# Kernel optimization log

Measured on AMD Instinct MI355X. Metric: run time of the kernel, lower is better.

## Reference

```python
import jax, jax.numpy as jnp
import numpy as np

N_USERS = 90000
N_ITEMS = 60000
N = N_USERS + N_ITEMS   # 150000 total nodes
D = 64                  # emb_dim
K = 128                 # n_intents
E = 1600000             # directed edges
L = 3                   # n_layers
EPS = 1e-12


def setup_inputs() -> dict:
    key = jax.random.key(0)
    k0, k1, k2, k3, k4 = jax.random.split(key, 5)
    embeddings = jax.random.normal(k0, (N, D), dtype=jnp.float32) * 0.1
    user_intent = jax.random.normal(k1, (D, K), dtype=jnp.float32) * 0.1
    item_intent = jax.random.normal(k2, (D, K), dtype=jnp.float32) * 0.1
    all_h = jax.random.randint(k3, (E,), 0, N, dtype=jnp.int32)
    all_t = jax.random.randint(k4, (E,), 0, N, dtype=jnp.int32)
    return {"embeddings": embeddings, "user_intent": user_intent,
            "item_intent": item_intent, "all_h": all_h, "all_t": all_t}


def _spmm(vals, h, t, x):
    # y[i] = sum_{e: h[e]==i} vals[e] * x[t[e]]   (sparse adj @ x)
    return jax.ops.segment_sum(vals[:, None] * x[t], h, num_segments=N)


def _sym_norm_values(h, t):
    # G = D^{-1/2} A D^{-1/2} edge values (A has unit edge weights)
    deg = jax.ops.segment_sum(jnp.ones((E,), jnp.float32), h, num_segments=N)
    d_inv = jnp.where(deg > 0, deg ** -0.5, 0.0)
    return d_inv[h] * d_inv[t]


def _adaptive_values(head_emb, tail_emb, h):
    # F.normalize: x / max(||x||, eps)
    hn = head_emb / jnp.maximum(jnp.linalg.norm(head_emb, axis=1, keepdims=True), EPS)
    tn = tail_emb / jnp.maximum(jnp.linalg.norm(tail_emb, axis=1, keepdims=True), EPS)
    edge_alpha = (jnp.sum(hn * tn, axis=1) + 1.0) * 0.5          # [E]
    row_sum = jax.ops.segment_sum(edge_alpha, h, num_segments=N)  # degree scores
    d_inv = jnp.where(row_sum > 0, 1.0 / row_sum, 0.0)           # pow(-1).nan_to_num
    return d_inv[h] * edge_alpha


def reference(embeddings, user_intent, item_intent, all_h, all_t):
    g_vals = _sym_norm_values(all_h, all_t)
    x = embeddings
    acc = x  # sum over all layer embeddings (incl. layer 0)
    for _ in range(L):
        gnn = _spmm(g_vals, all_h, all_t, x)
        u, it = x[:N_USERS], x[N_USERS:]
        u_int = jax.nn.softmax(u @ user_intent, axis=1) @ user_intent.T
        i_int = jax.nn.softmax(it @ item_intent, axis=1) @ item_intent.T
        intl = jnp.concatenate([u_int, i_int], axis=0)            # [N, D]
        gaa_vals = _adaptive_values(gnn[all_h], gnn[all_t], all_h)
        iaa_vals = _adaptive_values(intl[all_h], intl[all_t], all_h)
        gaa = _spmm(gaa_vals, all_h, all_t, x)
        iaa = _spmm(iaa_vals, all_h, all_t, x)
        x = gnn + intl + gaa + iaa + x
        acc = acc + x
    return acc
```

## Files before the change

### kernel.cpp

```cpp
#include <hip/hip_runtime.h>

#define N_USERS 90000
#define N_ITEMS 60000
#define NN      (N_USERS + N_ITEMS)
#define D       64
#define KDIM    128
#define NE      1600000
#define EPSF    1e-12f
#define ROWD    64
#define TU      ((N_USERS + 63) / 64)
#define TI      ((N_ITEMS + 63) / 64)
#define NINT    (TU + TI)
#define GB      4096


typedef __fp16 h2 __attribute__((ext_vector_type(2)));
typedef __fp16 h8 __attribute__((ext_vector_type(8)));
typedef float  f2 __attribute__((ext_vector_type(2)));
typedef float  f4v __attribute__((ext_vector_type(4)));

__device__ inline h2 as_h2(unsigned u) {
    union { unsigned u; h2 h; } v; v.u = u; return v.h;
}
__device__ inline h8 as_h8(uint4 u) {
    union { uint4 u; h8 h; } v; v.u = u; return v.h;
}
__device__ inline unsigned pkrtz(float a, float b) {
    auto r = __builtin_amdgcn_cvt_pkrtz(a, b);
    union { decltype(r) h; unsigned u; } v; v.h = r; return v.u;
}
__device__ inline f2 dec8lo(unsigned u) {
    return __builtin_amdgcn_cvt_pk_f32_fp8((int)u, false);
}
__device__ inline f2 dec8hi(unsigned u) {
    return __builtin_amdgcn_cvt_pk_f32_fp8((int)u, true);
}
__device__ inline unsigned enc8(float a, float b, float c, float d) {
    int u = __builtin_amdgcn_cvt_pk_fp8_f32(a, b, 0, false);
    u = __builtin_amdgcn_cvt_pk_fp8_f32(c, d, u, true);
    return (unsigned)u;
}


#define EB   ((NE + 255) / 256)
#define IB   ((NN * 16 + 255) / 256)
#define PREG (EB + IB + 16)

__global__ void k_pre(const int* __restrict__ h, int* __restrict__ deg,
                      const float* __restrict__ emb,
                      float* __restrict__ acc, unsigned* __restrict__ pkA,
                      const float* __restrict__ Wu, const float* __restrict__ Wi,
                      uint4* __restrict__ WfA, uint4* __restrict__ Wf2) {
    int bid = blockIdx.x;
    if (bid < EB) {
        int e = bid * 256 + threadIdx.x;
        if (e < NE) atomicAdd(&deg[h[e]], 1);
    } else if (bid < EB + IB) {
        int i = (bid - EB) * 256 + threadIdx.x;
        if (i >= NN * 16) return;
        float4 v = ((const float4*)emb)[i];
        ((float4*)acc)[i] = v;
        int row = i >> 4, l = i & 15;
        *(uint2*)&pkA[(size_t)row * ROWD + 32 + 2 * l] =
            make_uint2(pkrtz(v.x, v.y), pkrtz(v.z, v.w));
    } else {
        int i = (bid - EB - IB) * 256 + threadIdx.x;
        if (i >= 4096) return;
        int ph  = i >> 11;
        int r   = i & 2047;
        int mat = r >> 10;
        int rr  = r & 1023;
        const float* W = mat ? Wi : Wu;
        union { __fp16 hh[8]; uint4 u; } pkt;
        if (!ph) {
            int nt = rr >> 7, ks = (rr >> 6) & 1, lane = rr & 63;
            int q = lane >> 4, c = lane & 15;
            #pragma unroll
            for (int j = 0; j < 8; ++j)
                pkt.hh[j] = (__fp16)W[(32 * ks + 8 * q + j) * KDIM + nt * 16 + c];
            WfA[((mat * 8 + nt) * 2 + ks) * 64 + lane] = pkt.u;
        } else {
            int nt = rr >> 8, ks = (rr >> 6) & 3, lane = rr & 63;
            int q = lane >> 4, c = lane & 15;
            #pragma unroll
            for (int j = 0; j < 8; ++j)
                pkt.hh[j] = (__fp16)W[(nt * 16 + c) * KDIM + 32 * ks + 8 * q + j];
            Wf2[((mat * 4 + nt) * 4 + ks) * 64 + lane] = pkt.u;
        }
    }
}

__global__ void k_rowoff(const int* __restrict__ deg, int* __restrict__ counter,
                         int* __restrict__ row_off, int2* __restrict__ rodeg,
                         float* __restrict__ d_inv) {
    int i = blockIdx.x * blockDim.x + threadIdx.x;
    if (i >= NN) return;
    int d = deg[i];
    int ro = atomicAdd(counter, d);
    row_off[i] = ro;
    rodeg[i]   = make_int2(ro, d);
    d_inv[i]   = (d > 0) ? rsqrtf((float)d) : 0.f;
}

__global__ void k_scatter(const int* __restrict__ h, const int* __restrict__ t,
                          const int* __restrict__ row_off, int* __restrict__ row_cur,
                          const float* __restrict__ d_inv,
                          int2* __restrict__ csr) {
    int e = blockIdx.x * blockDim.x + threadIdx.x;
    if (e >= NE) return;
    int hh = h[e], tt = t[e];
    int slot = row_off[hh] + atomicAdd(&row_cur[hh], 1);
    csr[slot] = make_int2(tt, __float_as_int(d_inv[hh] * d_inv[tt]));
}

__global__ __launch_bounds__(256) void k_mid(const int2* __restrict__ rodeg,
                                             const int2* __restrict__ csr,
                                             unsigned* __restrict__ pk,
                                             unsigned* __restrict__ intl_h,
                                             const uint4* __restrict__ WfA,
                                             const uint4* __restrict__ Wf2,
                                             unsigned* __restrict__ base16) {
    __shared__ unsigned Plds[4096];
    int tid = threadIdx.x;
    int bid = blockIdx.x;

    if (bid < NINT) {
        int mat, bse, count, n0;
        if (bid < TU) { mat = 0; bse = 0;       count = N_USERS; n0 = bid * 64; }
        else          { mat = 1; bse = N_USERS; count = N_ITEMS; n0 = (bid - TU) * 64; }

        int wv = tid >> 6, la = tid & 63;
        int q = la >> 4, c = la & 15;

        int nA = n0 + wv * 16 + c;
        size_t gA = (size_t)min(bse + nA, NN - 1);
        const unsigned* prA = pk + gA * ROWD;
        uint4 a0u = *(const uint4*)&prA[32 + 4 * q];
        uint4 a1u = *(const uint4*)&prA[48 + 4 * q];

        f4v S[8];
        #pragma unroll
        for (int nt = 0; nt < 8; ++nt) S[nt] = (f4v){0.f, 0.f, 0.f, 0.f};
        const uint4* WA = WfA + (size_t)mat * 1024;
        #pragma unroll
        for (int nt = 0; nt < 8; ++nt) {
            h8 B0 = as_h8(WA[(nt * 2 + 0) * 64 + la]);
            h8 B1 = as_h8(WA[(nt * 2 + 1) * 64 + la]);
            S[nt] = __builtin_amdgcn_mfma_f32_16x16x32_f16(as_h8(a0u), B0, S[nt], 0, 0, 0);
            S[nt] = __builtin_amdgcn_mfma_f32_16x16x32_f16(as_h8(a1u), B1, S[nt], 0, 0, 0);
        }

        float inv_s[4];
        #pragma unroll
        for (int reg = 0; reg < 4; ++reg) {
            float m = S[0][reg];
            #pragma unroll
            for (int nt = 1; nt < 8; ++nt) m = fmaxf(m, S[nt][reg]);
            m = fmaxf(m, __shfl_xor(m, 1)); m = fmaxf(m, __shfl_xor(m, 2));
            m = fmaxf(m, __shfl_xor(m, 4)); m = fmaxf(m, __shfl_xor(m, 8));
            float sm = 0.f;
            #pragma unroll
            for (int nt = 0; nt < 8; ++nt) {
                float e_ = __expf(S[nt][reg] - m);
                S[nt][reg] = e_;
                sm += e_;
            }
            sm += __shfl_xor(sm, 1); sm += __shfl_xor(sm, 2);
            sm += __shfl_xor(sm, 4); sm += __shfl_xor(sm, 8);
            inv_s[reg] = 1.f / sm;
        }

        #pragma unroll
        for (int reg = 0; reg < 4; ++reg) {
            int ln = wv * 16 + q * 4 + reg;
            #pragma unroll
            for (int nt = 0; nt < 8; ++nt) {
                float v  = S[nt][reg] * inv_s[reg];
                float v1 = __shfl_xor(v, 1);
                if (!(c & 1)) {
                    int byte_in_row = nt * 32 + c * 2;
                    int sw = byte_in_row ^ ((ln & 7) << 4);
                    *(unsigned*)((char*)Plds + ln * 256 + sw) = pkrtz(v, v1);
                }
            }
        }

        f4v O[4];
        #pragma unroll
        for (int nt = 0; nt < 4; ++nt) O[nt] = (f4v){0.f, 0.f, 0.f, 0.f};
        const uint4* W2 = Wf2 + (size_t)mat * 1024;
        int lnA = wv * 16 + c;
        #pragma unroll
        for (int ks = 0; ks < 4; ++ks) {
            int byte_in_row = (32 * ks + 8 * q) * 2;
            int sw = byte_in_row ^ ((lnA & 7) << 4);
            uint4 au = *(const uint4*)((char*)Plds + lnA * 256 + sw);
            #pragma unroll
            for (int nt = 0; nt < 4; ++nt) {
                h8 Bp = as_h8(W2[(nt * 4 + ks) * 64 + la]);
                O[nt] = __builtin_amdgcn_mfma_f32_16x16x32_f16(as_h8(au), Bp, O[nt], 0, 0, 0);
            }
        }

        #pragma unroll
        for (int reg = 0; reg < 4; ++reg) {
            float ss = 0.f;
            #pragma unroll
            for (int nt = 0; nt < 4; ++nt) ss = fmaf(O[nt][reg], O[nt][reg], ss);
            ss += __shfl_xor(ss, 1); ss += __shfl_xor(ss, 2);
            ss += __shfl_xor(ss, 4); ss += __shfl_xor(ss, 8);
            float invn = 1.f / fmaxf(sqrtf(ss), EPSF);
            int n = n0 + wv * 16 + q * 4 + reg;
            bool valid = n < count;
            size_t g = (size_t)(bse + n);
            #pragma unroll
            for (int nt = 0; nt < 4; ++nt) {
                float v  = O[nt][reg];
                float v1 = __shfl_xor(v, 1);
                float v2 = __shfl_xor(v, 2);
                float v3 = __shfl_xor(v, 3);
                if (valid) {
                    if (!(c & 1))
                        intl_h[g * 32 + ((nt * 16 + c) >> 1)] = pkrtz(v, v1);
                    if (!(c & 3))
                        pk[g * ROWD + 2 * ((nt * 16 + c) >> 2) + 1] =
                            enc8(v * invn, v1 * invn, v2 * invn, v3 * invn);
                }
            }
        }
    } else {
        int lane = tid & 63;
        int grp = lane >> 3, l8 = lane & 7;
        int nw = GB * 4;
        for (int wid = (bid - NINT) * 4 + (tid >> 6); wid < NN; wid += nw) {
            int2 rd = rodeg[wid];
            int s = rd.x, eend = rd.x + rd.y;
            float a0 = 0.f, a1 = 0.f, a2 = 0.f, a3 = 0.f;
            float a4 = 0.f, a5 = 0.f, a6 = 0.f, a7 = 0.f;
            int e = s;
            int2 c  = csr[min(s + grp, eend - 1)];
            uint4 w = *(const uint4*)&pk[(size_t)c.x * ROWD + 32 + 4 * l8];
            int2 c1 = csr[min(s + 8 + grp, eend - 1)];
            for (; e + 7 < eend; e += 8) {
                int2 c2  = csr[min(e + 16 + grp, eend - 1)];
                uint4 w1 = *(const uint4*)&pk[(size_t)c1.x * ROWD + 32 + 4 * l8];
                float gv = __int_as_float(c.y);
                h2 x0 = as_h2(w.x), x1 = as_h2(w.y), x2 = as_h2(w.z), x3 = as_h2(w.w);
                a0 = fmaf(gv, (float)x0.x, a0); a1 = fmaf(gv, (float)x0.y, a1);
                a2 = fmaf(gv, (float)x1.x, a2); a3 = fmaf(gv, (float)x1.y, a3);
                a4 = fmaf(gv, (float)x2.x, a4); a5 = fmaf(gv, (float)x2.y, a5);
                a6 = fmaf(gv, (float)x3.x, a6); a7 = fmaf(gv, (float)x3.y, a7);
                c = c1; c1 = c2; w = w1;
            }
            if (e < eend) {
                bool val = e + grp < eend;
                float gv = val ? __int_as_float(c.y) : 0.f;
                h2 x0 = as_h2(w.x), x1 = as_h2(w.y), x2 = as_h2(w.z), x3 = as_h2(w.w);
                a0 = fmaf(gv, (float)x0.x, a0); a1 = fmaf(gv, (float)x0.y, a1);
                a2 = fmaf(gv, (float)x1.x, a2); a3 = fmaf(gv, (float)x1.y, a3);
                a4 = fmaf(gv, (float)x2.x, a4); a5 = fmaf(gv, (float)x2.y, a5);
                a6 = fmaf(gv, (float)x3.x, a6); a7 = fmaf(gv, (float)x3.y, a7);
            }
            #pragma unroll
            for (int m = 8; m <= 32; m <<= 1) {
                a0 += __shfl_xor(a0, m); a1 += __shfl_xor(a1, m);
                a2 += __shfl_xor(a2, m); a3 += __shfl_xor(a3, m);
                a4 += __shfl_xor(a4, m); a5 += __shfl_xor(a5, m);
                a6 += __shfl_xor(a6, m); a7 += __shfl_xor(a7, m);
            }
            float ss = fmaf(a0, a0, fmaf(a1, a1, fmaf(a2, a2, a3 * a3)))
                     + fmaf(a4, a4, fmaf(a5, a5, fmaf(a6, a6, a7 * a7)));
            ss += __shfl_xor(ss, 1); ss += __shfl_xor(ss, 2); ss += __shfl_xor(ss, 4);
            float inv = 1.f / fmaxf(sqrtf(ss), EPSF);
            if (grp == 0) {
                unsigned* pr = pk + (size_t)wid * ROWD;
                pr[4 * l8]     = enc8(a0 * inv, a1 * inv, a2 * inv, a3 * inv);
                pr[4 * l8 + 2] = enc8(a4 * inv, a5 * inv, a6 * inv, a7 * inv);
                uint4 xw = *(const uint4*)&pr[32 + 4 * l8];
                h2 x0 = as_h2(xw.x), x1 = as_h2(xw.y), x2 = as_h2(xw.z), x3 = as_h2(xw.w);
                *(uint4*)&base16[(size_t)wid * 32 + 4 * l8] = make_uint4(
                    pkrtz(a0 + (float)x0.x, a1 + (float)x0.y),
                    pkrtz(a2 + (float)x1.x, a3 + (float)x1.y),
                    pkrtz(a4 + (float)x2.x, a5 + (float)x2.y),
                    pkrtz(a6 + (float)x3.x, a7 + (float)x3.y));
            }
        }
    }
}

__global__ __launch_bounds__(256) void k_fused(const int2* __restrict__ rodeg,
                                               const int2* __restrict__ csr,
                                               const unsigned* __restrict__ pk,
                                               const unsigned* __restrict__ intl_h,
                                               const unsigned* __restrict__ base16,
                                               unsigned* __restrict__ pknext,
                                               float* __restrict__ acc) {
    int lane = threadIdx.x & 63;
    int grp = lane >> 4, l16 = lane & 15;
    int nw = GB * 4;
    for (int wid = blockIdx.x * 4 + (threadIdx.x >> 6); wid < NN; wid += nw) {
        const unsigned* ph = pk + (size_t)wid * ROWD;
        uint2 hq = *(const uint2*)&ph[2 * l16];
        f2 hgl = dec8lo(hq.x), hgh = dec8hi(hq.x);
        f2 hil = dec8lo(hq.y), hih = dec8hi(hq.y);

        int2 rd = rodeg[wid];
        int s = rd.x, eend = rd.x + rd.y;
        float sg = 0.f, si = 0.f;
        float g0 = 0.f, g1 = 0.f, g2 = 0.f, g3 = 0.f;
        float i0 = 0.f, i1 = 0.f, i2 = 0.f, i3 = 0.f;

        int e = s;
        int tA = csr[min(s + grp, eend - 1)].x;
        int tB = csr[min(s + 4 + grp, eend - 1)].x;
        const unsigned* pA = pk + (size_t)tA * ROWD;
        const unsigned* pB = pk + (size_t)tB * ROWD;
        uint2 qA = *(const uint2*)&pA[2 * l16];
        uint2 wA = *(const uint2*)&pA[32 + 2 * l16];
        uint2 qB = *(const uint2*)&pB[2 * l16];
        uint2 wB = *(const uint2*)&pB[32 + 2 * l16];
        int tA1 = csr[min(s + 8 + grp, eend - 1)].x;
        int tB1 = csr[min(s + 12 + grp, eend - 1)].x;

        for (; e + 7 < eend; e += 8) {
            int tA2 = csr[min(e + 16 + grp, eend - 1)].x;
            int tB2 = csr[min(e + 20 + grp, eend - 1)].x;
            const unsigned* pA1 = pk + (size_t)tA1 * ROWD;
            const unsigned* pB1 = pk + (size_t)tB1 * ROWD;
            uint2 qA1 = *(const uint2*)&pA1[2 * l16];
            uint2 wA1 = *(const uint2*)&pA1[32 + 2 * l16];
            uint2 qB1 = *(const uint2*)&pB1[2 * l16];
            uint2 wB1 = *(const uint2*)&pB1[32 + 2 * l16];
            f2 gA01 = dec8lo(qA.x), gA23 = dec8hi(qA.x);
            f2 iA01 = dec8lo(qA.y), iA23 = dec8hi(qA.y);
            f2 gB01 = dec8lo(qB.x), gB23 = dec8hi(qB.x);
            f2 iB01 = dec8lo(qB.y), iB23 = dec8hi(qB.y);
            float pgA = fmaf(hgl.x, gA01.x, fmaf(hgl.y, gA01.y,
                        fmaf(hgh.x, gA23.x, hgh.y * gA23.y)));
            float piA = fmaf(hil.x, iA01.x, fmaf(hil.y, iA01.y,
                        fmaf(hih.x, iA23.x, hih.y * iA23.y)));
            float pgB = fmaf(hgl.x, gB01.x, fmaf(hgl.y, gB01.y,
                        fmaf(hgh.x, gB23.x, hgh.y * gB23.y)));
            float piB = fmaf(hil.x, iB01.x, fmaf(hil.y, iB01.y,
                        fmaf(hih.x, iB23.x, hih.y * iB23.y)));
            #pragma unroll
            for (int m = 1; m <= 8; m <<= 1) {
                pgA += __shfl_xor(pgA, m); piA += __shfl_xor(piA, m);
                pgB += __shfl_xor(pgB, m); piB += __shfl_xor(piB, m);
            }
            float agA = fmaf(pgA, 0.5f, 0.5f), aiA = fmaf(piA, 0.5f, 0.5f);
            float agB = fmaf(pgB, 0.5f, 0.5f), aiB = fmaf(piB, 0.5f, 0.5f);
            sg += agA + agB; si += aiA + aiB;
            h2 xa0 = as_h2(wA.x), xa1 = as_h2(wA.y);
            h2 xb0 = as_h2(wB.x), xb1 = as_h2(wB.y);
            g0 = fmaf(agA, (float)xa0.x, g0); g1 = fmaf(agA, (float)xa0.y, g1);
            g2 = fmaf(agA, (float)xa1.x, g2); g3 = fmaf(agA, (float)xa1.y, g3);
            i0 = fmaf(aiA, (float)xa0.x, i0); i1 = fmaf(aiA, (float)xa0.y, i1);
            i2 = fmaf(aiA, (float)xa1.x, i2); i3 = fmaf(aiA, (float)xa1.y, i3);
            g0 = fmaf(agB, (float)xb0.x, g0); g1 = fmaf(agB, (float)xb0.y, g1);
            g2 = fmaf(agB, (float)xb1.x, g2); g3 = fmaf(agB, (float)xb1.y, g3);
            i0 = fmaf(aiB, (float)xb0.x, i0); i1 = fmaf(aiB, (float)xb0.y, i1);
            i2 = fmaf(aiB, (float)xb1.x, i2); i3 = fmaf(aiB, (float)xb1.y, i3);
            tA1 = tA2; tB1 = tB2;
            qA = qA1; wA = wA1; qB = qB1; wB = wB1;
        }
        if (e < eend) {
            bool val = e + grp < eend;
            f2 tg01 = dec8lo(qA.x), tg23 = dec8hi(qA.x);
            f2 ti01 = dec8lo(qA.y), ti23 = dec8hi(qA.y);
            float pg = fmaf(hgl.x, tg01.x, fmaf(hgl.y, tg01.y,
                       fmaf(hgh.x, tg23.x, hgh.y * tg23.y)));
            float pi = fmaf(hil.x, ti01.x, fmaf(hil.y, ti01.y,
                       fmaf(hih.x, ti23.x, hih.y * ti23.y)));
            #pragma unroll
            for (int m = 1; m <= 8; m <<= 1) {
                pg += __shfl_xor(pg, m); pi += __shfl_xor(pi, m);
            }
            float ag = fmaf(pg, 0.5f, 0.5f), ai = fmaf(pi, 0.5f, 0.5f);
            if (!val) { ag = 0.f; ai = 0.f; }
            sg += ag; si += ai;
            h2 x0 = as_h2(wA.x), x1 = as_h2(wA.y);
            g0 = fmaf(ag, (float)x0.x, g0); g1 = fmaf(ag, (float)x0.y, g1);
            g2 = fmaf(ag, (float)x1.x, g2); g3 = fmaf(ag, (float)x1.y, g3);
            i0 = fmaf(ai, (float)x0.x, i0); i1 = fmaf(ai, (float)x0.y, i1);
            i2 = fmaf(ai, (float)x1.x, i2); i3 = fmaf(ai, (float)x1.y, i3);
        }
        if (e + 4 < eend) {
            bool val = e + 4 + grp < eend;
            f2 tg01 = dec8lo(qB.x), tg23 = dec8hi(qB.x);
            f2 ti01 = dec8lo(qB.y), ti23 = dec8hi(qB.y);
            float pg = fmaf(hgl.x, tg01.x, fmaf(hgl.y, tg01.y,
                       fmaf(hgh.x, tg23.x, hgh.y * tg23.y)));
            float pi = fmaf(hil.x, ti01.x, fmaf(hil.y, ti01.y,
                       fmaf(hih.x, ti23.x, hih.y * ti23.y)));
            #pragma unroll
            for (int m = 1; m <= 8; m <<= 1) {
                pg += __shfl_xor(pg, m); pi += __shfl_xor(pi, m);
            }
            float ag = fmaf(pg, 0.5f, 0.5f), ai = fmaf(pi, 0.5f, 0.5f);
            if (!val) { ag = 0.f; ai = 0.f; }
            sg += ag; si += ai;
            h2 x0 = as_h2(wB.x), x1 = as_h2(wB.y);
            g0 = fmaf(ag, (float)x0.x, g0); g1 = fmaf(ag, (float)x0.y, g1);
            g2 = fmaf(ag, (float)x1.x, g2); g3 = fmaf(ag, (float)x1.y, g3);
            i0 = fmaf(ai, (float)x0.x, i0); i1 = fmaf(ai, (float)x0.y, i1);
            i2 = fmaf(ai, (float)x1.x, i2); i3 = fmaf(ai, (float)x1.y, i3);
        }

        #pragma unroll
        for (int m = 16; m <= 32; m <<= 1) {
            sg += __shfl_xor(sg, m); si += __shfl_xor(si, m);
            g0 += __shfl_xor(g0, m); g1 += __shfl_xor(g1, m);
            g2 += __shfl_xor(g2, m); g3 += __shfl_xor(g3, m);
            i0 += __shfl_xor(i0, m); i1 += __shfl_xor(i1, m);
            i2 += __shfl_xor(i2, m); i3 += __shfl_xor(i3, m);
        }

        if (grp == 0) {
            float invg = sg > 0.f ? 1.f / sg : 0.f;
            float invi = si > 0.f ? 1.f / si : 0.f;
            size_t bidx = (size_t)wid * 16 + l16;
            uint2 bw = *(const uint2*)&base16[(size_t)wid * 32 + 2 * l16];
            h2 b0 = as_h2(bw.x), b1 = as_h2(bw.y);
            uint2 iw = *(const uint2*)&intl_h[(size_t)wid * 32 + 2 * l16];
            h2 il0 = as_h2(iw.x), il1 = as_h2(iw.y);
            float o0 = (float)b0.x + (float)il0.x + invg * g0 + invi * i0;
            float o1 = (float)b0.y + (float)il0.y + invg * g1 + invi * i1;
            float o2 = (float)b1.x + (float)il1.x + invg * g2 + invi * i2;
            float o3 = (float)b1.y + (float)il1.y + invg * g3 + invi * i3;
            *(uint2*)&pknext[(size_t)wid * ROWD + 32 + 2 * l16] =
                make_uint2(pkrtz(o0, o1), pkrtz(o2, o3));
            float4 a = ((float4*)acc)[bidx];
            a.x += o0; a.y += o1; a.z += o2; a.w += o3;
            ((float4*)acc)[bidx] = a;
        }
    }
}


extern "C" void kernel_launch(void* const* d_in, const int* in_sizes, int n_in,
                              void* d_out, int out_size, void* d_ws, size_t ws_size,
                              hipStream_t stream) {
    const float* emb   = (const float*)d_in[0];
    const float* Wu    = (const float*)d_in[1];
    const float* Wi    = (const float*)d_in[2];
    const int*   all_h = (const int*)d_in[3];
    const int*   all_t = (const int*)d_in[4];
    float*       acc   = (float*)d_out;

    char*  bp  = (char*)d_ws;
    size_t off = 0;
    auto take = [&](size_t bytes) -> char* {
        char* r = bp + off;
        off = (off + bytes + 255) & ~(size_t)255;
        return r;
    };
    int*      deg     = (int*)     take((size_t)NN * 4);
    int*      row_off = (int*)     take((size_t)NN * 4);
    int2*     rodeg   = (int2*)    take((size_t)NN * 8);
    int*      row_cur = (int*)     take((size_t)NN * 4);
    int*      counter = (int*)     take(256);
    float*    d_inv   = (float*)   take((size_t)NN * 4);
    int2*     csr     = (int2*)    take((size_t)NE * 8);
    unsigned* pkA     = (unsigned*)take((size_t)NN * ROWD * 4);
    unsigned* pkB     = (unsigned*)take((size_t)NN * ROWD * 4);
    unsigned* intl_h  = (unsigned*)take((size_t)NN * 32 * 4);
    unsigned* base16  = (unsigned*)take((size_t)NN * 32 * 4);
    uint4*    WfA     = (uint4*)   take((size_t)2048 * 16);
    uint4*    Wf2     = (uint4*)   take((size_t)2048 * 16);
    (void)ws_size; (void)in_sizes; (void)n_in; (void)out_size;

    hipMemsetAsync(deg, 0, (size_t)NN * 4, stream);
    hipMemsetAsync(row_cur, 0, (size_t)NN * 4, stream);
    hipMemsetAsync(counter, 0, 256, stream);

    const int NBK = (NN + 255) / 256;
    k_pre<<<PREG, 256, 0, stream>>>(all_h, deg, emb, acc, pkA, Wu, Wi, WfA, Wf2);
    k_rowoff<<<NBK, 256, 0, stream>>>(deg, counter, row_off, rodeg, d_inv);
    k_scatter<<<EB, 256, 0, stream>>>(all_h, all_t, row_off, row_cur, d_inv, csr);

    unsigned* cur = pkA;
    unsigned* nxt = pkB;
    for (int l = 0; l < 3; ++l) {
        k_mid<<<NINT + GB, 256, 0, stream>>>(rodeg, csr, cur, intl_h,
                                             WfA, Wf2, base16);
        k_fused<<<GB, 256, 0, stream>>>(rodeg, csr, cur, intl_h,
                                        base16, nxt, acc);
        unsigned* tmp = cur; cur = nxt; nxt = tmp;
    }
}
```

Before: 786.3 us.

## Defer fp32 accumulator to a final pass and use compact target-index array

```diff
diff --git a/kernel.cpp b/kernel.cpp
--- a/kernel.cpp
+++ b/kernel.cpp
@@ -48,7 +48,7 @@
 
 __global__ void k_pre(const int* __restrict__ h, int* __restrict__ deg,
                       const float* __restrict__ emb,
-                      float* __restrict__ acc, unsigned* __restrict__ pkA,
+                      unsigned* __restrict__ pkA,
                       const float* __restrict__ Wu, const float* __restrict__ Wi,
                       uint4* __restrict__ WfA, uint4* __restrict__ Wf2) {
     int bid = blockIdx.x;
@@ -59,7 +59,6 @@
         int i = (bid - EB) * 256 + threadIdx.x;
         if (i >= NN * 16) return;
         float4 v = ((const float4*)emb)[i];
-        ((float4*)acc)[i] = v;
         int row = i >> 4, l = i & 15;
         *(uint2*)&pkA[(size_t)row * ROWD + 32 + 2 * l] =
             make_uint2(pkrtz(v.x, v.y), pkrtz(v.z, v.w));
@@ -105,12 +104,33 @@
 __global__ void k_scatter(const int* __restrict__ h, const int* __restrict__ t,
                           const int* __restrict__ row_off, int* __restrict__ row_cur,
                           const float* __restrict__ d_inv,
-                          int2* __restrict__ csr) {
+                          int2* __restrict__ csr, int* __restrict__ tarr) {
     int e = blockIdx.x * blockDim.x + threadIdx.x;
     if (e >= NE) return;
     int hh = h[e], tt = t[e];
     int slot = row_off[hh] + atomicAdd(&row_cur[hh], 1);
-    csr[slot] = make_int2(tt, __float_as_int(d_inv[hh] * d_inv[tt]));
+    csr[slot]  = make_int2(tt, __float_as_int(d_inv[hh] * d_inv[tt]));
+    tarr[slot] = tt;
+}
+
+__global__ void k_acc(const float* __restrict__ emb, const unsigned* __restrict__ xs1,
+                      const unsigned* __restrict__ pkA_, const unsigned* __restrict__ pkB_,
+                      float* __restrict__ acc) {
+    int i = blockIdx.x * blockDim.x + threadIdx.x;
+    if (i >= NN * 16) return;
+    int row = i >> 4, l = i & 15;
+    float4 v = ((const float4*)emb)[i];
+    uint2 u1 = *(const uint2*)&xs1[(size_t)row * 32 + 2 * l];
+    uint2 u2 = *(const uint2*)&pkA_[(size_t)row * ROWD + 32 + 2 * l];
+    uint2 u3 = *(const uint2*)&pkB_[(size_t)row * ROWD + 32 + 2 * l];
+    h2 a1 = as_h2(u1.x), b1 = as_h2(u1.y);
+    h2 a2 = as_h2(u2.x), b2 = as_h2(u2.y);
+    h2 a3 = as_h2(u3.x), b3 = as_h2(u3.y);
+    v.x += (float)a1.x + (float)a2.x + (float)a3.x;
+    v.y += (float)a1.y + (float)a2.y + (float)a3.y;
+    v.z += (float)b1.x + (float)b2.x + (float)b3.x;
+    v.w += (float)b1.y + (float)b2.y + (float)b3.y;
+    ((float4*)acc)[i] = v;
 }
 
 __global__ __launch_bounds__(256) void k_mid(const int2* __restrict__ rodeg,
@@ -289,12 +309,13 @@
 }
 
 __global__ __launch_bounds__(256) void k_fused(const int2* __restrict__ rodeg,
-                                               const int2* __restrict__ csr,
+                                               const int* __restrict__ tarr,
                                                const unsigned* __restrict__ pk,
                                                const unsigned* __restrict__ intl_h,
                                                const unsigned* __restrict__ base16,
                                                unsigned* __restrict__ pknext,
-                                               float* __restrict__ acc) {
+                                               unsigned* __restrict__ xsave,
+                                               int save1) {
     int lane = threadIdx.x & 63;
     int grp = lane >> 4, l16 = lane & 15;
     int nw = GB * 4;
@@ -311,20 +332,20 @@
         float i0 = 0.f, i1 = 0.f, i2 = 0.f, i3 = 0.f;
 
         int e = s;
-        int tA = csr[min(s + grp, eend - 1)].x;
-        int tB = csr[min(s + 4 + grp, eend - 1)].x;
+        int tA = tarr[min(s + grp, eend - 1)];
+        int tB = tarr[min(s + 4 + grp, eend - 1)];
         const unsigned* pA = pk + (size_t)tA * ROWD;
         const unsigned* pB = pk + (size_t)tB * ROWD;
         uint2 qA = *(const uint2*)&pA[2 * l16];
         uint2 wA = *(const uint2*)&pA[32 + 2 * l16];
         uint2 qB = *(const uint2*)&pB[2 * l16];
         uint2 wB = *(const uint2*)&pB[32 + 2 * l16];
-        int tA1 = csr[min(s + 8 + grp, eend - 1)].x;
-        int tB1 = csr[min(s + 12 + grp, eend - 1)].x;
+        int tA1 = tarr[min(s + 8 + grp, eend - 1)];
+        int tB1 = tarr[min(s + 12 + grp, eend - 1)];
 
         for (; e + 7 < eend; e += 8) {
-            int tA2 = csr[min(e + 16 + grp, eend - 1)].x;
-            int tB2 = csr[min(e + 20 + grp, eend - 1)].x;
+            int tA2 = tarr[min(e + 16 + grp, eend - 1)];
+            int tB2 = tarr[min(e + 20 + grp, eend - 1)];
             const unsigned* pA1 = pk + (size_t)tA1 * ROWD;
             const unsigned* pB1 = pk + (size_t)tB1 * ROWD;
             uint2 qA1 = *(const uint2*)&pA1[2 * l16];
@@ -419,7 +440,6 @@
         if (grp == 0) {
             float invg = sg > 0.f ? 1.f / sg : 0.f;
             float invi = si > 0.f ? 1.f / si : 0.f;
-            size_t bidx = (size_t)wid * 16 + l16;
             uint2 bw = *(const uint2*)&base16[(size_t)wid * 32 + 2 * l16];
             h2 b0 = as_h2(bw.x), b1 = as_h2(bw.y);
             uint2 iw = *(const uint2*)&intl_h[(size_t)wid * 32 + 2 * l16];
@@ -428,11 +448,10 @@
             float o1 = (float)b0.y + (float)il0.y + invg * g1 + invi * i1;
             float o2 = (float)b1.x + (float)il1.x + invg * g2 + invi * i2;
             float o3 = (float)b1.y + (float)il1.y + invg * g3 + invi * i3;
-            *(uint2*)&pknext[(size_t)wid * ROWD + 32 + 2 * l16] =
-                make_uint2(pkrtz(o0, o1), pkrtz(o2, o3));
-            float4 a = ((float4*)acc)[bidx];
-            a.x += o0; a.y += o1; a.z += o2; a.w += o3;
-            ((float4*)acc)[bidx] = a;
+            uint2 px = make_uint2(pkrtz(o0, o1), pkrtz(o2, o3));
+            *(uint2*)&pknext[(size_t)wid * ROWD + 32 + 2 * l16] = px;
+            if (save1)
+                *(uint2*)&xsave[(size_t)wid * 32 + 2 * l16] = px;
         }
     }
 }
@@ -462,10 +481,12 @@
     int*      counter = (int*)     take(256);
     float*    d_inv   = (float*)   take((size_t)NN * 4);
     int2*     csr     = (int2*)    take((size_t)NE * 8);
+    int*      tarr    = (int*)     take((size_t)NE * 4);
     unsigned* pkA     = (unsigned*)take((size_t)NN * ROWD * 4);
     unsigned* pkB     = (unsigned*)take((size_t)NN * ROWD * 4);
     unsigned* intl_h  = (unsigned*)take((size_t)NN * 32 * 4);
     unsigned* base16  = (unsigned*)take((size_t)NN * 32 * 4);
+    unsigned* xs1     = (unsigned*)take((size_t)NN * 32 * 4);
     uint4*    WfA     = (uint4*)   take((size_t)2048 * 16);
     uint4*    Wf2     = (uint4*)   take((size_t)2048 * 16);
     (void)ws_size; (void)in_sizes; (void)n_in; (void)out_size;
@@ -475,17 +496,18 @@
     hipMemsetAsync(counter, 0, 256, stream);
 
     const int NBK = (NN + 255) / 256;
-    k_pre<<<PREG, 256, 0, stream>>>(all_h, deg, emb, acc, pkA, Wu, Wi, WfA, Wf2);
+    k_pre<<<PREG, 256, 0, stream>>>(all_h, deg, emb, pkA, Wu, Wi, WfA, Wf2);
     k_rowoff<<<NBK, 256, 0, stream>>>(deg, counter, row_off, rodeg, d_inv);
-    k_scatter<<<EB, 256, 0, stream>>>(all_h, all_t, row_off, row_cur, d_inv, csr);
+    k_scatter<<<EB, 256, 0, stream>>>(all_h, all_t, row_off, row_cur, d_inv, csr, tarr);
 
     unsigned* cur = pkA;
     unsigned* nxt = pkB;
     for (int l = 0; l < 3; ++l) {
         k_mid<<<NINT + GB, 256, 0, stream>>>(rodeg, csr, cur, intl_h,
                                              WfA, Wf2, base16);
-        k_fused<<<GB, 256, 0, stream>>>(rodeg, csr, cur, intl_h,
-                                        base16, nxt, acc);
+        k_fused<<<GB, 256, 0, stream>>>(rodeg, tarr, cur, intl_h,
+                                        base16, nxt, xs1, l == 0 ? 1 : 0);
         unsigned* tmp = cur; cur = nxt; nxt = tmp;
     }
-}
+    k_acc<<<IB, 256, 0, stream>>>(emb, xs1, pkA, pkB, acc);
+}
```

After: 794.5 us. No clear change (+1.0%).
